# Kernel optimization log

Measured on AMD Instinct MI355X. Metric: run time of the kernel, lower is better.

## Reference

```python
import jax, jax.numpy as jnp
import numpy as np

HEAD_NUM = 8
EMB = 256
HEAD_SIZE = EMB // HEAD_NUM
POS_LEN = 128
ROPE_BASE = 100.0
LN_EPS = 1e-5
SOFTPICK_EPS = 1e-6


def _rope_tables():
    inv_freq = 1.0 / ROPE_BASE ** (jnp.arange(0, HEAD_SIZE, 2, dtype=jnp.float32) / HEAD_SIZE)
    t = jnp.arange(POS_LEN, dtype=jnp.float32)
    freqs = jnp.einsum('i,j->ij', t, inv_freq)          # [W, hs/2]
    freqs = jnp.concatenate([freqs, freqs], axis=-1)     # [W, hs]
    return jnp.sin(freqs), jnp.cos(freqs)


def _apply_rope(e, sin, cos):
    # e: [..., W, hs]; sin/cos: [W, hs]
    h = HEAD_SIZE // 2
    rot = jnp.concatenate([-e[..., h:], e[..., :h]], axis=-1)
    return e * cos + rot * sin


def _layernorm(x, g, b):
    mu = jnp.mean(x, axis=-1, keepdims=True)
    var = jnp.mean(jnp.square(x - mu), axis=-1, keepdims=True)
    return (x - mu) * jax.lax.rsqrt(var + LN_EPS) * g + b


def _softpick(x):
    m = jnp.max(x, axis=-1, keepdims=True)
    e = jnp.exp(x - m) - jnp.exp(-m)
    return jax.nn.relu(e) / (jnp.sum(jnp.abs(e), axis=-1, keepdims=True) + SOFTPICK_EPS)


def setup_inputs() -> dict:
    key = jax.random.key(0)
    ks = jax.random.split(key, 12)
    B, C, H, W = 4, EMB, 256, 128
    hn, hs = HEAD_NUM, HEAD_SIZE
    s = 0.02
    return {
        'left': jax.random.normal(ks[0], (B, C, H, W), jnp.float32),
        'right': jax.random.normal(ks[1], (B, C, H, W), jnp.float32),
        'qw': jax.random.normal(ks[2], (hn, hs, hs), jnp.float32) * s,   # grouped 1x1 conv weights
        'kw': jax.random.normal(ks[3], (hn, hs, hs), jnp.float32) * s,
        'vw': jax.random.normal(ks[4], (hn, hs, hs), jnp.float32) * s,
        'proj_w': jax.random.normal(ks[5], (C, C), jnp.float32) * s,
        'proj_b': jnp.zeros((C,), jnp.float32),
        'ln1_g': jnp.ones((C,), jnp.float32),
        'ln1_b': jnp.zeros((C,), jnp.float32),
        'ln2_g': jnp.ones((C,), jnp.float32),
        'ln2_b': jnp.zeros((C,), jnp.float32),
        'w1': jax.random.normal(ks[6], (C, 4 * C), jnp.float32) * s,
        'b1': jnp.zeros((4 * C,), jnp.float32),
        'w2': jax.random.normal(ks[7], (4 * C, C), jnp.float32) * s,
        'b2': jnp.zeros((C,), jnp.float32),
    }


def reference(left, right, qw, kw, vw, proj_w, proj_b,
              ln1_g, ln1_b, ln2_g, ln2_b, w1, b1, w2, b2):
    B, C, H, W = left.shape
    hn, hs = HEAD_NUM, HEAD_SIZE
    scale = hs ** -0.5
    sin, cos = _rope_tables()  # [W, hs]

    def grouped_proj(x, w):
        # grouped 1x1 conv -> per-head matmul; out [B, H, hn, W, hs]
        xr = x.reshape(B, hn, hs, H, W)
        return jnp.einsum('bgihw,goi->bhgwo', xr, w)

    q = _apply_rope(grouped_proj(left, qw), sin, cos)
    k = _apply_rope(grouped_proj(right, kw), sin, cos)
    v = grouped_proj(right, vw)

    att = _softpick(jnp.einsum('bhgqd,bhgkd->bhgqk', q, k) * scale)  # [B,H,hn,W,W]
    out = jnp.einsum('bhgqk,bhgkd->bhqgd', att, v).reshape(B, H, W, C)

    x1 = _layernorm(out @ proj_w + proj_b + jnp.transpose(left, (0, 2, 3, 1)), ln1_g, ln1_b)
    ffn = jax.nn.gelu(x1 @ w1 + b1, approximate=False) @ w2 + b2
    return _layernorm(ffn + x1, ln2_g, ln2_b)
```

## Files before the change

kernel.cpp:

```cpp
#include <hip/hip_runtime.h>
#include <hip/hip_bf16.h>

#define DEV __device__ __forceinline__

typedef __attribute__((ext_vector_type(8))) short bf16x8_t;
typedef __attribute__((ext_vector_type(4))) float f32x4_t;

constexpr int cB = 4, cC = 256, cH = 256, cW = 128, cHN = 8, cHS = 32;
constexpr int cM = cB * cH * cW;

DEV float bfu(unsigned int b16) { union { unsigned int u; float f; } v; v.u = b16 << 16; return v.f; }
DEV unsigned short f2bb(float f) { union { __hip_bfloat16 h; unsigned short u; } v; v.h = __float2bfloat16(f); return v.u; }
DEV unsigned int pk2(float a, float b) { return (unsigned)f2bb(a) | ((unsigned)f2bb(b) << 16); }

#define GLOAD_LDS16(g, l) \
  __builtin_amdgcn_global_load_lds((const __attribute__((address_space(1))) void*)(g), \
                                   (__attribute__((address_space(3))) void*)(l), 16, 0, 0)

DEV float gelu_fast(float v) {
  float ax = fabsf(v) * 0.7071067811865475f;
  float t = __builtin_amdgcn_rcpf(1.0f + 0.3275911f * ax);
  float poly = ((((1.061405429f * t - 1.453152027f) * t + 1.421413741f) * t
                 - 0.284496736f) * t + 0.254829592f) * t;
  float e = __expf(-ax * ax);
  float erfv = 1.0f - poly * e;
  float phi = 0.5f + 0.5f * copysignf(erfv, v);
  return v * phi;
}

__global__ __launch_bounds__(256) void transpose_bf16(const float* __restrict__ src,
                                                      __hip_bfloat16* __restrict__ dst,
                                                      int R, int Ccol) {
  int idx = blockIdx.x * 256 + threadIdx.x;
  if (idx < R * Ccol) {
    int r = idx / Ccol, c = idx - r * Ccol;
    dst[c * R + r] = __float2bfloat16(src[idx]);
  }
}

__global__ __launch_bounds__(256) void transpose_perm_fp8(const float* __restrict__ src,
                                                          unsigned char* __restrict__ dst,
                                                          int R, int Ccol) {
  int idx = blockIdx.x * 256 + threadIdx.x;
  if (idx < R * Ccol) {
    int r = idx / Ccol, c = idx - r * Ccol;
    int pk = (r & ~255) | ((r & 15) << 4) | ((r >> 4) & 15);
    int u = __builtin_amdgcn_cvt_pk_fp8_f32(src[idx] * 64.0f, 0.0f, 0, false);
    dst[(size_t)c * R + pk] = (unsigned char)(u & 0xff);
  }
}

__global__ __launch_bounds__(256) void rope_init(float2* __restrict__ tab) {
  int i = blockIdx.x * 256 + threadIdx.x;
  int w = i >> 4, c = i & 15;
  float inv = expf((float)c * -0.28782313662425572f);
  float ang = (float)w * inv;
  tab[i] = make_float2(sinf(ang), cosf(ang));
}

constexpr int XL_OFF = 0, XR_OFF = 10240, WQ_OFF = 20480, WK_OFF = 23040, WV_OFF = 25600;
constexpr int QS_OFF = 28160, KS_OFF = 38400, VT_OFF = 0, P_OFF = 10240;
constexpr int SMEM_BYTES = 48640;

__global__ __launch_bounds__(256) void attn_mfma(
    const float* __restrict__ left, const float* __restrict__ right,
    const float* __restrict__ qw, const float* __restrict__ kw, const float* __restrict__ vw,
    const float2* __restrict__ rope,
    __hip_bfloat16* __restrict__ att_out)
{
  __shared__ __align__(16) char smem[SMEM_BYTES];

  const int t = threadIdx.x;
  const int g = blockIdx.x & 7;
  const int h = (blockIdx.x >> 3) & 255;
  const int b = blockIdx.x >> 11;
  const size_t HW = (size_t)cH * cW;

  {
    const float* lb = left  + ((size_t)(b * cC + g * cHS) * cH + h) * cW;
    const float* rb = right + ((size_t)(b * cC + g * cHS) * cH + h) * cW;
    int w = t & 127, ih = (t >> 7) * 16;
    unsigned short* xlrow = (unsigned short*)(smem + XL_OFF) + w * 40 + ih;
    unsigned short* xrrow = (unsigned short*)(smem + XR_OFF) + w * 40 + ih;
#pragma unroll
    for (int i = 0; i < 16; i += 2) {
      float a0 = lb[(size_t)(ih + i) * HW + w], a1 = lb[(size_t)(ih + i + 1) * HW + w];
      *(unsigned int*)(xlrow + i) = pk2(a0, a1);
      float c0 = rb[(size_t)(ih + i) * HW + w], c1 = rb[(size_t)(ih + i + 1) * HW + w];
      *(unsigned int*)(xrrow + i) = pk2(c0, c1);
    }
    int o = t >> 3, i0 = (t & 7) * 4;
    {
      float4 v4 = *(const float4*)(qw + g * 1024 + t * 4);
      unsigned short* dst = (unsigned short*)(smem + WQ_OFF) + o * 40 + i0;
      *(unsigned int*)(dst) = pk2(v4.x, v4.y); *(unsigned int*)(dst + 2) = pk2(v4.z, v4.w);
    }
    {
      float4 v4 = *(const float4*)(kw + g * 1024 + t * 4);
      unsigned short* dst = (unsigned short*)(smem + WK_OFF) + o * 40 + i0;
      *(unsigned int*)(dst) = pk2(v4.x, v4.y); *(unsigned int*)(dst + 2) = pk2(v4.z, v4.w);
    }
    {
      float4 v4 = *(const float4*)(vw + g * 1024 + t * 4);
      unsigned short* dst = (unsigned short*)(smem + WV_OFF) + o * 40 + i0;
      *(unsigned int*)(dst) = pk2(v4.x, v4.y); *(unsigned int*)(dst + 2) = pk2(v4.z, v4.w);
    }
  }
  __syncthreads();

  const int lane = t & 63, wid = t >> 6;
  const int c = lane & 15, q4 = lane >> 4;
  const int wbase = wid * 32;
  const f32x4_t zero = {0.f, 0.f, 0.f, 0.f};

  bf16x8_t a_xl[2], a_xr[2];
#pragma unroll
  for (int sub = 0; sub < 2; ++sub) {
    a_xl[sub] = *(const bf16x8_t*)(smem + XL_OFF + (wbase + sub * 16 + c) * 80 + q4 * 16);
    a_xr[sub] = *(const bf16x8_t*)(smem + XR_OFF + (wbase + sub * 16 + c) * 80 + q4 * 16);
  }
  f32x4_t qacc[2][2], kacc[2][2];
#pragma unroll
  for (int ot = 0; ot < 2; ++ot) {
    bf16x8_t bq = *(const bf16x8_t*)(smem + WQ_OFF + (ot * 16 + c) * 80 + q4 * 16);
    bf16x8_t bk = *(const bf16x8_t*)(smem + WK_OFF + (ot * 16 + c) * 80 + q4 * 16);
#pragma unroll
    for (int sub = 0; sub < 2; ++sub) {
      qacc[sub][ot] = __builtin_amdgcn_mfma_f32_16x16x32_bf16(a_xl[sub], bq, zero, 0, 0, 0);
      kacc[sub][ot] = __builtin_amdgcn_mfma_f32_16x16x32_bf16(a_xr[sub], bk, zero, 0, 0, 0);
    }
  }
  {
    const float scale = 0.17677669529663687f;
    unsigned short* qsp = (unsigned short*)(smem + QS_OFF);
    unsigned short* ksp = (unsigned short*)(smem + KS_OFF);
#pragma unroll
    for (int sub = 0; sub < 2; ++sub)
#pragma unroll
      for (int r = 0; r < 4; ++r) {
        int w = wbase + sub * 16 + q4 * 4 + r;
        float2 sc = rope[w * 16 + c];
        float sn = sc.x, cs = sc.y;
        float q0 = qacc[sub][0][r], q1 = qacc[sub][1][r];
        qsp[w * 40 + c]      = f2bb((q0 * cs - q1 * sn) * scale);
        qsp[w * 40 + c + 16] = f2bb((q1 * cs + q0 * sn) * scale);
        float k0 = kacc[sub][0][r], k1 = kacc[sub][1][r];
        ksp[w * 40 + c]      = f2bb(k0 * cs - k1 * sn);
        ksp[w * 40 + c + 16] = f2bb(k1 * cs + k0 * sn);
      }
  }
  __syncthreads();

  {
    f32x4_t vacc[2][2];
#pragma unroll
    for (int dt = 0; dt < 2; ++dt) {
      bf16x8_t awv = *(const bf16x8_t*)(smem + WV_OFF + (dt * 16 + c) * 80 + q4 * 16);
#pragma unroll
      for (int sub = 0; sub < 2; ++sub)
        vacc[dt][sub] = __builtin_amdgcn_mfma_f32_16x16x32_bf16(awv, a_xr[sub], zero, 0, 0, 0);
    }
    unsigned short* vtp = (unsigned short*)(smem + VT_OFF);
#pragma unroll
    for (int dt = 0; dt < 2; ++dt)
#pragma unroll
      for (int r = 0; r < 4; ++r) {
        int d = dt * 16 + q4 * 4 + r;
        *(unsigned int*)(vtp + d * 136 + c * 8 + wid * 2) = pk2(vacc[dt][0][r], vacc[dt][1][r]);
      }
  }

  bf16x8_t aq0 = *(const bf16x8_t*)(smem + QS_OFF + (wbase + c) * 80 + q4 * 16);
  bf16x8_t aq1 = *(const bf16x8_t*)(smem + QS_OFF + (wbase + 16 + c) * 80 + q4 * 16);
  f32x4_t sac[2][8];
#pragma unroll
  for (int kt = 0; kt < 8; ++kt) {
    bf16x8_t bk = *(const bf16x8_t*)(smem + KS_OFF + (kt * 16 + c) * 80 + q4 * 16);
    sac[0][kt] = __builtin_amdgcn_mfma_f32_16x16x32_bf16(aq0, bk, zero, 0, 0, 0);
    sac[1][kt] = __builtin_amdgcn_mfma_f32_16x16x32_bf16(aq1, bk, zero, 0, 0, 0);
  }

  float dinv_[2][4];
#pragma unroll
  for (int sub = 0; sub < 2; ++sub)
#pragma unroll
    for (int r = 0; r < 4; ++r) {
      float m = sac[sub][0][r];
#pragma unroll
      for (int kt = 1; kt < 8; ++kt) m = fmaxf(m, sac[sub][kt][r]);
      m = fmaxf(m, __shfl_xor(m, 1));
      m = fmaxf(m, __shfl_xor(m, 2));
      m = fmaxf(m, __shfl_xor(m, 4));
      m = fmaxf(m, __shfl_xor(m, 8));
      float em = __expf(-m);
      float ss = 0.f;
#pragma unroll
      for (int kt = 0; kt < 8; ++kt) {
        float e = __expf(sac[sub][kt][r] - m) - em;
        sac[sub][kt][r] = fmaxf(e, 0.f);
        ss += fabsf(e);
      }
      ss += __shfl_xor(ss, 1);
      ss += __shfl_xor(ss, 2);
      ss += __shfl_xor(ss, 4);
      ss += __shfl_xor(ss, 8);
      dinv_[sub][r] = 1.0f / (ss + 1e-6f);
    }
  __syncthreads();

  {
    unsigned short* pp = (unsigned short*)(smem + P_OFF);
#pragma unroll
    for (int sub = 0; sub < 2; ++sub)
#pragma unroll
      for (int r = 0; r < 4; ++r) {
        int w = wbase + sub * 16 + q4 * 4 + r;
        float dv = dinv_[sub][r];
        uint4 u;
        u.x = pk2(sac[sub][0][r] * dv, sac[sub][1][r] * dv);
        u.y = pk2(sac[sub][2][r] * dv, sac[sub][3][r] * dv);
        u.z = pk2(sac[sub][4][r] * dv, sac[sub][5][r] * dv);
        u.w = pk2(sac[sub][6][r] * dv, sac[sub][7][r] * dv);
        *(uint4*)(pp + w * 136 + c * 8) = u;
      }
  }
  f32x4_t oacc[2][2] = {{zero, zero}, {zero, zero}};
#pragma unroll
  for (int ks = 0; ks < 4; ++ks) {
    bf16x8_t ap0 = *(const bf16x8_t*)(smem + P_OFF + (wbase + c) * 272 + ks * 64 + q4 * 16);
    bf16x8_t ap1 = *(const bf16x8_t*)(smem + P_OFF + (wbase + 16 + c) * 272 + ks * 64 + q4 * 16);
    bf16x8_t bv0 = *(const bf16x8_t*)(smem + VT_OFF + (c) * 272 + ks * 64 + q4 * 16);
    bf16x8_t bv1 = *(const bf16x8_t*)(smem + VT_OFF + (16 + c) * 272 + ks * 64 + q4 * 16);
    oacc[0][0] = __builtin_amdgcn_mfma_f32_16x16x32_bf16(ap0, bv0, oacc[0][0], 0, 0, 0);
    oacc[0][1] = __builtin_amdgcn_mfma_f32_16x16x32_bf16(ap0, bv1, oacc[0][1], 0, 0, 0);
    oacc[1][0] = __builtin_amdgcn_mfma_f32_16x16x32_bf16(ap1, bv0, oacc[1][0], 0, 0, 0);
    oacc[1][1] = __builtin_amdgcn_mfma_f32_16x16x32_bf16(ap1, bv1, oacc[1][1], 0, 0, 0);
  }
  {
    __hip_bfloat16* ob = att_out + ((size_t)(b * cH + h) * cW) * cC + g * cHS;
#pragma unroll
    for (int sub = 0; sub < 2; ++sub)
#pragma unroll
      for (int dt = 0; dt < 2; ++dt)
#pragma unroll
        for (int r = 0; r < 4; ++r) {
          int w = wbase + sub * 16 + q4 * 4 + r;
          ob[(size_t)w * cC + dt * 16 + c] = __float2bfloat16(oacc[sub][dt][r]);
        }
  }
}

__global__ __launch_bounds__(256, 2) void proj_gemm_ln(
    const __hip_bfloat16* __restrict__ A, const __hip_bfloat16* __restrict__ Bt,
    const float* __restrict__ bias, const float* __restrict__ leftres,
    const float* __restrict__ g, const float* __restrict__ be,
    __hip_bfloat16* __restrict__ outp)
{
  constexpr int KK = 256;
  __shared__ __align__(16) char smem[73728];
  const int t = threadIdx.x, lane = t & 63, wid = t >> 6;
  const int c = lane & 15, q4 = lane >> 4;
  const int m0 = blockIdx.x * 128;
  const int wr = wid * 32;
  const f32x4_t zero = {0.f, 0.f, 0.f, 0.f};

  f32x4_t acc[2][16];
#pragma unroll
  for (int fi = 0; fi < 2; ++fi)
#pragma unroll
    for (int fj = 0; fj < 16; ++fj) acc[fi][fj] = zero;

  auto stage = [&](int buf, int k0) {
    char* As = smem + buf * 24576;
    char* Bs = As + 8192;
#pragma unroll
    for (int i = 0; i < 2; ++i) {
      int chunk = (wid * 2 + i);
      int row = chunk * 16 + (lane >> 2);
      int sw = (((lane & 3) ^ ((row >> 1) & 3))) * 8;
      GLOAD_LDS16(A + (size_t)(m0 + row) * KK + k0 + sw, As + chunk * 1024);
    }
#pragma unroll
    for (int i = 0; i < 4; ++i) {
      int chunk = (wid * 4 + i);
      int row = chunk * 16 + (lane >> 2);
      int sw = (((lane & 3) ^ ((row >> 1) & 3))) * 8;
      GLOAD_LDS16(Bt + (size_t)row * KK + k0 + sw, Bs + chunk * 1024);
    }
  };

  constexpr int NK = KK >> 5;
  stage(0, 0);
  stage(1, 32);
  for (int tt = 0; tt < NK; ++tt) {
    if (tt + 2 < NK) {
      stage((tt + 2) % 3, (tt + 2) << 5);
      asm volatile("s_waitcnt vmcnt(12)" ::: "memory");
    } else if (tt + 1 < NK) {
      asm volatile("s_waitcnt vmcnt(6)" ::: "memory");
    } else {
      asm volatile("s_waitcnt vmcnt(0)" ::: "memory");
    }
    __builtin_amdgcn_s_barrier();
    __builtin_amdgcn_sched_barrier(0);
    char* As = smem + (tt % 3) * 24576;
    char* Bs = As + 8192;
    int ra0 = wr + c, ra1 = wr + 16 + c;
    bf16x8_t af0 = *(const bf16x8_t*)(As + ra0 * 64 + ((q4 ^ ((ra0 >> 1) & 3)) * 16));
    bf16x8_t af1 = *(const bf16x8_t*)(As + ra1 * 64 + ((q4 ^ ((ra1 >> 1) & 3)) * 16));
#pragma unroll
    for (int fj = 0; fj < 16; ++fj) {
      int rb = fj * 16 + c;
      bf16x8_t bf = *(const bf16x8_t*)(Bs + rb * 64 + ((q4 ^ ((rb >> 1) & 3)) * 16));
      acc[0][fj] = __builtin_amdgcn_mfma_f32_16x16x32_bf16(af0, bf, acc[0][fj], 0, 0, 0);
      acc[1][fj] = __builtin_amdgcn_mfma_f32_16x16x32_bf16(af1, bf, acc[1][fj], 0, 0, 0);
    }
    __builtin_amdgcn_sched_barrier(0);
    __builtin_amdgcn_s_barrier();
  }

  {
    const int b_ = m0 >> 15, h_ = (m0 >> 7) & 255;
#pragma unroll
    for (int fj = 0; fj < 16; ++fj) {
      int n = fj * 16 + c;
      float bv = bias[n];
#pragma unroll
      for (int fi = 0; fi < 2; ++fi) {
        int w0 = wr + fi * 16 + q4 * 4;
        float4 lr = *(const float4*)(leftres + (((size_t)b_ * 256 + n) * 256 + h_) * 128 + w0);
        float la[4] = {lr.x, lr.y, lr.z, lr.w};
#pragma unroll
        for (int r = 0; r < 4; ++r) acc[fi][fj][r] += bv + la[r];
      }
    }
  }

  float mu[2][4], rs[2][4];
#pragma unroll
  for (int fi = 0; fi < 2; ++fi)
#pragma unroll
    for (int r = 0; r < 4; ++r) {
      float s = 0.f;
#pragma unroll
      for (int fj = 0; fj < 16; ++fj) s += acc[fi][fj][r];
      s += __shfl_xor(s, 1); s += __shfl_xor(s, 2); s += __shfl_xor(s, 4); s += __shfl_xor(s, 8);
      float m_ = s * (1.0f / 256.0f);
      float sq = 0.f;
#pragma unroll
      for (int fj = 0; fj < 16; ++fj) { float d = acc[fi][fj][r] - m_; sq += d * d; }
      sq += __shfl_xor(sq, 1); sq += __shfl_xor(sq, 2); sq += __shfl_xor(sq, 4); sq += __shfl_xor(sq, 8);
      mu[fi][r] = m_;
      rs[fi][r] = rsqrtf(sq * (1.0f / 256.0f) + 1e-5f);
    }
#pragma unroll
  for (int fj = 0; fj < 16; ++fj) {
    int n = fj * 16 + c;
    float gv = g[n], bev = be[n];
#pragma unroll
    for (int fi = 0; fi < 2; ++fi)
#pragma unroll
      for (int r = 0; r < 4; ++r) {
        int row = wr + fi * 16 + q4 * 4 + r;
        outp[(size_t)(m0 + row) * 256 + n] =
            __float2bfloat16((acc[fi][fj][r] - mu[fi][r]) * rs[fi][r] * gv + bev);
      }
  }
}

__global__ __launch_bounds__(256, 2) void ffn1_wide(
    const __hip_bfloat16* __restrict__ A, const __hip_bfloat16* __restrict__ Bt,
    const float* __restrict__ bias, unsigned char* __restrict__ outb)
{
  constexpr int KK = 256, N = 1024;
  __shared__ __align__(16) char smem[73728];
  const int t = threadIdx.x, lane = t & 63, wid = t >> 6;
  const int c = lane & 15, q4 = lane >> 4;
  const int mb = blockIdx.x & 1023, nc = blockIdx.x >> 10;
  const int m0 = mb * 128, n0 = nc * 256;
  const int wr = wid * 32;
  const f32x4_t zero = {0.f, 0.f, 0.f, 0.f};

  f32x4_t acc[2][16];
#pragma unroll
  for (int fi = 0; fi < 2; ++fi)
#pragma unroll
    for (int fj = 0; fj < 16; ++fj) acc[fi][fj] = zero;

  const __hip_bfloat16* Bbase = Bt + (size_t)n0 * KK;

  auto stage = [&](int buf, int k0) {
    char* As = smem + buf * 24576;
    char* Bs = As + 8192;
#pragma unroll
    for (int i = 0; i < 2; ++i) {
      int chunk = (wid * 2 + i);
      int row = chunk * 16 + (lane >> 2);
      int sw = (((lane & 3) ^ ((row >> 1) & 3))) * 8;
      GLOAD_LDS16(A + (size_t)(m0 + row) * KK + k0 + sw, As + chunk * 1024);
    }
#pragma unroll
    for (int i = 0; i < 4; ++i) {
      int chunk = (wid * 4 + i);
      int row = chunk * 16 + (lane >> 2);
      int sw = (((lane & 3) ^ ((row >> 1) & 3))) * 8;
      GLOAD_LDS16(Bbase + (size_t)row * KK + k0 + sw, Bs + chunk * 1024);
    }
  };

  constexpr int NK = KK >> 5;
  stage(0, 0);
  stage(1, 32);
  for (int tt = 0; tt < NK; ++tt) {
    if (tt + 2 < NK) {
      stage((tt + 2) % 3, (tt + 2) << 5);
      asm volatile("s_waitcnt vmcnt(12)" ::: "memory");
    } else if (tt + 1 < NK) {
      asm volatile("s_waitcnt vmcnt(6)" ::: "memory");
    } else {
      asm volatile("s_waitcnt vmcnt(0)" ::: "memory");
    }
    __builtin_amdgcn_s_barrier();
    __builtin_amdgcn_sched_barrier(0);
    char* As = smem + (tt % 3) * 24576;
    char* Bs = As + 8192;
    int ra0 = wr + c, ra1 = wr + 16 + c;
    bf16x8_t af0 = *(const bf16x8_t*)(As + ra0 * 64 + ((q4 ^ ((ra0 >> 1) & 3)) * 16));
    bf16x8_t af1 = *(const bf16x8_t*)(As + ra1 * 64 + ((q4 ^ ((ra1 >> 1) & 3)) * 16));
#pragma unroll
    for (int fj = 0; fj < 16; ++fj) {
      int rb = fj * 16 + c;
      bf16x8_t bf = *(const bf16x8_t*)(Bs + rb * 64 + ((q4 ^ ((rb >> 1) & 3)) * 16));
      acc[0][fj] = __builtin_amdgcn_mfma_f32_16x16x32_bf16(af0, bf, acc[0][fj], 0, 0, 0);
      acc[1][fj] = __builtin_amdgcn_mfma_f32_16x16x32_bf16(af1, bf, acc[1][fj], 0, 0, 0);
    }
    __builtin_amdgcn_sched_barrier(0);
    __builtin_amdgcn_s_barrier();
  }

  float bv[16];
#pragma unroll
  for (int fj = 0; fj < 16; ++fj) bv[fj] = bias[n0 + fj * 16 + c];
  unsigned char* obase = outb + (size_t)(m0 + wr + q4 * 4) * N + n0 + c * 16;
#pragma unroll
  for (int fi = 0; fi < 2; ++fi)
#pragma unroll
    for (int r = 0; r < 4; ++r) {
      uint4 u;
      unsigned int* up = (unsigned int*)&u;
#pragma unroll
      for (int p = 0; p < 4; ++p) {
        float v0 = gelu_fast(acc[fi][4 * p + 0][r] + bv[4 * p + 0]) * 64.0f;
        float v1 = gelu_fast(acc[fi][4 * p + 1][r] + bv[4 * p + 1]) * 64.0f;
        float v2 = gelu_fast(acc[fi][4 * p + 2][r] + bv[4 * p + 2]) * 64.0f;
        float v3 = gelu_fast(acc[fi][4 * p + 3][r] + bv[4 * p + 3]) * 64.0f;
        int w = __builtin_amdgcn_cvt_pk_fp8_f32(v0, v1, 0, false);
        w = __builtin_amdgcn_cvt_pk_fp8_f32(v2, v3, w, true);
        up[p] = (unsigned)w;
      }
      *(uint4*)(obase + (size_t)(fi * 16 + r) * N) = u;
    }
}

__global__ __launch_bounds__(256, 2) void ffn2_ln(
    const unsigned char* __restrict__ A, const unsigned char* __restrict__ Bt,
    const float* __restrict__ bias, const __hip_bfloat16* __restrict__ resbf,
    const float* __restrict__ g, const float* __restrict__ be,
    float* __restrict__ outp)
{
  constexpr int KK = 1024;
  __shared__ __align__(16) char smem[73728];
  const int t = threadIdx.x, lane = t & 63, wid = t >> 6;
  const int c = lane & 15, q4 = lane >> 4;
  const int m0 = blockIdx.x * 128;
  const int wr = wid * 32;
  const f32x4_t zero = {0.f, 0.f, 0.f, 0.f};

  f32x4_t acc[2][16];
#pragma unroll
  for (int fi = 0; fi < 2; ++fi)
#pragma unroll
    for (int fj = 0; fj < 16; ++fj) acc[fi][fj] = zero;

  auto stage = [&](int buf, int k0) {
    char* As = smem + buf * 24576;
    char* Bs = As + 8192;
#pragma unroll
    for (int i = 0; i < 2; ++i) {
      int chunk = (wid * 2 + i);
      int row = chunk * 16 + (lane >> 2);
      int sw = (((lane & 3) ^ ((row >> 1) & 3))) * 16;
      GLOAD_LDS16(A + (size_t)(m0 + row) * KK + k0 + sw, As + chunk * 1024);
    }
#pragma unroll
    for (int i = 0; i < 4; ++i) {
      int chunk = (wid * 4 + i);
      int row = chunk * 16 + (lane >> 2);
      int sw = (((lane & 3) ^ ((row >> 1) & 3))) * 16;
      GLOAD_LDS16(Bt + (size_t)row * KK + k0 + sw, Bs + chunk * 1024);
    }
  };

  constexpr int NK = 16;
  stage(0, 0);
  stage(1, 64);
  const int sl = (c >> 1) & 3;
  const int koff0 = ((((q4 >> 1)) ^ sl) << 4) | ((q4 & 1) << 3);
  const int koff1 = (((2 | (q4 >> 1)) ^ sl) << 4) | ((q4 & 1) << 3);
  for (int tt = 0; tt < NK; ++tt) {
    if (tt + 2 < NK) {
      stage((tt + 2) % 3, (tt + 2) << 6);
      asm volatile("s_waitcnt vmcnt(12)" ::: "memory");
    } else if (tt + 1 < NK) {
      asm volatile("s_waitcnt vmcnt(6)" ::: "memory");
    } else {
      asm volatile("s_waitcnt vmcnt(0)" ::: "memory");
    }
    __builtin_amdgcn_s_barrier();
    __builtin_amdgcn_sched_barrier(0);
    char* As = smem + (tt % 3) * 24576;
    char* Bs = As + 8192;
    const char* arow0 = As + (wr + c) * 64;
    const char* arow1 = As + (wr + 16 + c) * 64;
    long a00 = *(const long*)(arow0 + koff0);
    long a01 = *(const long*)(arow0 + koff1);
    long a10 = *(const long*)(arow1 + koff0);
    long a11 = *(const long*)(arow1 + koff1);
#pragma unroll
    for (int fj = 0; fj < 16; ++fj) {
      const char* brow = Bs + (fj * 16 + c) * 64;
      long b0 = *(const long*)(brow + koff0);
      long b1 = *(const long*)(brow + koff1);
      acc[0][fj] = __builtin_amdgcn_mfma_f32_16x16x32_fp8_fp8(a00, b0, acc[0][fj], 0, 0, 0);
      acc[0][fj] = __builtin_amdgcn_mfma_f32_16x16x32_fp8_fp8(a01, b1, acc[0][fj], 0, 0, 0);
      acc[1][fj] = __builtin_amdgcn_mfma_f32_16x16x32_fp8_fp8(a10, b0, acc[1][fj], 0, 0, 0);
      acc[1][fj] = __builtin_amdgcn_mfma_f32_16x16x32_fp8_fp8(a11, b1, acc[1][fj], 0, 0, 0);
    }
    __builtin_amdgcn_sched_barrier(0);
    __builtin_amdgcn_s_barrier();
  }

#pragma unroll
  for (int fj = 0; fj < 16; ++fj) {
    int n = fj * 16 + c;
    float bv = bias[n];
#pragma unroll
    for (int fi = 0; fi < 2; ++fi)
#pragma unroll
      for (int r = 0; r < 4; ++r) {
        int row = wr + fi * 16 + q4 * 4 + r;
        acc[fi][fj][r] = acc[fi][fj][r] * 0.000244140625f + bv +
                         __bfloat162float(resbf[(size_t)(m0 + row) * 256 + n]);
      }
  }

  float mu[2][4], rs[2][4];
#pragma unroll
  for (int fi = 0; fi < 2; ++fi)
#pragma unroll
    for (int r = 0; r < 4; ++r) {
      float s = 0.f;
#pragma unroll
      for (int fj = 0; fj < 16; ++fj) s += acc[fi][fj][r];
      s += __shfl_xor(s, 1); s += __shfl_xor(s, 2); s += __shfl_xor(s, 4); s += __shfl_xor(s, 8);
      float m_ = s * (1.0f / 256.0f);
      float sq = 0.f;
#pragma unroll
      for (int fj = 0; fj < 16; ++fj) { float d = acc[fi][fj][r] - m_; sq += d * d; }
      sq += __shfl_xor(sq, 1); sq += __shfl_xor(sq, 2); sq += __shfl_xor(sq, 4); sq += __shfl_xor(sq, 8);
      mu[fi][r] = m_;
      rs[fi][r] = rsqrtf(sq * (1.0f / 256.0f) + 1e-5f);
    }
#pragma unroll
  for (int fj = 0; fj < 16; ++fj) {
    int n = fj * 16 + c;
    float gv = g[n], bev = be[n];
#pragma unroll
    for (int fi = 0; fi < 2; ++fi)
#pragma unroll
      for (int r = 0; r < 4; ++r) {
        int row = wr + fi * 16 + q4 * 4 + r;
        outp[(size_t)(m0 + row) * 256 + n] =
            (acc[fi][fj][r] - mu[fi][r]) * rs[fi][r] * gv + bev;
      }
  }
}

extern "C" void kernel_launch(void* const* d_in, const int* in_sizes, int n_in,
                              void* d_out, int out_size, void* d_ws, size_t ws_size,
                              hipStream_t stream) {
  const float* left   = (const float*)d_in[0];
  const float* right  = (const float*)d_in[1];
  const float* qw     = (const float*)d_in[2];
  const float* kw     = (const float*)d_in[3];
  const float* vw     = (const float*)d_in[4];
  const float* proj_w = (const float*)d_in[5];
  const float* proj_b = (const float*)d_in[6];
  const float* ln1_g  = (const float*)d_in[7];
  const float* ln1_b  = (const float*)d_in[8];
  const float* ln2_g  = (const float*)d_in[9];
  const float* ln2_b  = (const float*)d_in[10];
  const float* w1     = (const float*)d_in[11];
  const float* b1     = (const float*)d_in[12];
  const float* w2     = (const float*)d_in[13];
  const float* b2     = (const float*)d_in[14];

  char* ws = (char*)d_ws;
  __hip_bfloat16* att_out = (__hip_bfloat16*)ws;
  __hip_bfloat16* x1      = (__hip_bfloat16*)(ws + 67108864);
  unsigned char*  hidden  = (unsigned char*)(ws + 134217728);
  float2*         rope    = (float2*)(ws + 301989888);
  __hip_bfloat16* pwT     = (__hip_bfloat16*)(ws + 402653184);
  __hip_bfloat16* w1T     = pwT + 65536;
  unsigned char*  w2T     = (unsigned char*)(w1T + 262144);

  transpose_bf16<<<256, 256, 0, stream>>>(proj_w, pwT, 256, 256);
  transpose_bf16<<<1024, 256, 0, stream>>>(w1, w1T, 256, 1024);
  transpose_perm_fp8<<<1024, 256, 0, stream>>>(w2, w2T, 1024, 256);
  rope_init<<<8, 256, 0, stream>>>(rope);

  attn_mfma<<<cB * cH * cHN, 256, 0, stream>>>(left, right, qw, kw, vw, rope, att_out);

  proj_gemm_ln<<<cM / 128, 256, 0, stream>>>(att_out, pwT, proj_b, left, ln1_g, ln1_b, x1);
  ffn1_wide<<<4096, 256, 0, stream>>>(x1, w1T, b1, hidden);
  ffn2_ln<<<cM / 128, 256, 0, stream>>>(hidden, w2T, b2, x1, ln2_g, ln2_b, (float*)d_out);
}
```

Measured before the change: 411.7 us.

## Load attention inputs directly into registers, use FP8 for PV, remap FFN1 blocks per XCD

```diff
diff --git a/kernel.cpp b/kernel.cpp
--- a/kernel.cpp
+++ b/kernel.cpp
@@ -58,9 +58,9 @@
   tab[i] = make_float2(sinf(ang), cosf(ang));
 }
 
-constexpr int XL_OFF = 0, XR_OFF = 10240, WQ_OFF = 20480, WK_OFF = 23040, WV_OFF = 25600;
-constexpr int QS_OFF = 28160, KS_OFF = 38400, VT_OFF = 0, P_OFF = 10240;
-constexpr int SMEM_BYTES = 48640;
+constexpr int WQ_OFF = 0, WK_OFF = 2560, WV_OFF = 5120, QS_OFF = 7680, KS_OFF = 17920;
+constexpr int VT_OFF = 28160, P_OFF = 0;
+constexpr int SMEM_BYTES = 32512;
 
 __global__ __launch_bounds__(256) void attn_mfma(
     const float* __restrict__ left, const float* __restrict__ right,
@@ -76,19 +76,35 @@
   const int b = blockIdx.x >> 11;
   const size_t HW = (size_t)cH * cW;
 
+  const int lane = t & 63, wid = t >> 6;
+  const int c = lane & 15, q4 = lane >> 4;
+  const int wbase = wid * 32;
+  const f32x4_t zero = {0.f, 0.f, 0.f, 0.f};
+
+  const float* lb = left  + ((size_t)(b * cC + g * cHS) * cH + h) * cW;
+  const float* rb = right + ((size_t)(b * cC + g * cHS) * cH + h) * cW;
+
+  bf16x8_t a_xl[2], a_xr[2];
+#pragma unroll
+  for (int sub = 0; sub < 2; ++sub) {
+    int w = wbase + sub * 16 + c;
+    float xl[8], xr[8];
+#pragma unroll
+    for (int e = 0; e < 8; ++e) {
+      xl[e] = lb[(size_t)(q4 * 8 + e) * HW + w];
+      xr[e] = rb[(size_t)(q4 * 8 + e) * HW + w];
+    }
+    union { bf16x8_t v; unsigned int u[4]; } ul, ur;
+#pragma unroll
+    for (int p = 0; p < 4; ++p) {
+      ul.u[p] = pk2(xl[2 * p], xl[2 * p + 1]);
+      ur.u[p] = pk2(xr[2 * p], xr[2 * p + 1]);
+    }
+    a_xl[sub] = ul.v;
+    a_xr[sub] = ur.v;
+  }
+
   {
-    const float* lb = left  + ((size_t)(b * cC + g * cHS) * cH + h) * cW;
-    const float* rb = right + ((size_t)(b * cC + g * cHS) * cH + h) * cW;
-    int w = t & 127, ih = (t >> 7) * 16;
-    unsigned short* xlrow = (unsigned short*)(smem + XL_OFF) + w * 40 + ih;
-    unsigned short* xrrow = (unsigned short*)(smem + XR_OFF) + w * 40 + ih;
-#pragma unroll
-    for (int i = 0; i < 16; i += 2) {
-      float a0 = lb[(size_t)(ih + i) * HW + w], a1 = lb[(size_t)(ih + i + 1) * HW + w];
-      *(unsigned int*)(xlrow + i) = pk2(a0, a1);
-      float c0 = rb[(size_t)(ih + i) * HW + w], c1 = rb[(size_t)(ih + i + 1) * HW + w];
-      *(unsigned int*)(xrrow + i) = pk2(c0, c1);
-    }
     int o = t >> 3, i0 = (t & 7) * 4;
     {
       float4 v4 = *(const float4*)(qw + g * 1024 + t * 4);
@@ -108,17 +124,6 @@
   }
   __syncthreads();
 
-  const int lane = t & 63, wid = t >> 6;
-  const int c = lane & 15, q4 = lane >> 4;
-  const int wbase = wid * 32;
-  const f32x4_t zero = {0.f, 0.f, 0.f, 0.f};
-
-  bf16x8_t a_xl[2], a_xr[2];
-#pragma unroll
-  for (int sub = 0; sub < 2; ++sub) {
-    a_xl[sub] = *(const bf16x8_t*)(smem + XL_OFF + (wbase + sub * 16 + c) * 80 + q4 * 16);
-    a_xr[sub] = *(const bf16x8_t*)(smem + XR_OFF + (wbase + sub * 16 + c) * 80 + q4 * 16);
-  }
   f32x4_t qacc[2][2], kacc[2][2];
 #pragma unroll
   for (int ot = 0; ot < 2; ++ot) {
@@ -160,13 +165,15 @@
       for (int sub = 0; sub < 2; ++sub)
         vacc[dt][sub] = __builtin_amdgcn_mfma_f32_16x16x32_bf16(awv, a_xr[sub], zero, 0, 0, 0);
     }
-    unsigned short* vtp = (unsigned short*)(smem + VT_OFF);
+    unsigned char* vtp = (unsigned char*)(smem + VT_OFF);
 #pragma unroll
     for (int dt = 0; dt < 2; ++dt)
 #pragma unroll
       for (int r = 0; r < 4; ++r) {
         int d = dt * 16 + q4 * 4 + r;
-        *(unsigned int*)(vtp + d * 136 + c * 8 + wid * 2) = pk2(vacc[dt][0][r], vacc[dt][1][r]);
+        int u = __builtin_amdgcn_cvt_pk_fp8_f32(vacc[dt][0][r] * 16.0f,
+                                                vacc[dt][1][r] * 16.0f, 0, false);
+        *(unsigned short*)(vtp + d * 136 + c * 8 + wid * 2) = (unsigned short)(u & 0xffff);
       }
   }
 
@@ -209,32 +216,33 @@
   __syncthreads();
 
   {
-    unsigned short* pp = (unsigned short*)(smem + P_OFF);
+    unsigned char* pp = (unsigned char*)(smem + P_OFF);
 #pragma unroll
     for (int sub = 0; sub < 2; ++sub)
 #pragma unroll
       for (int r = 0; r < 4; ++r) {
         int w = wbase + sub * 16 + q4 * 4 + r;
-        float dv = dinv_[sub][r];
-        uint4 u;
-        u.x = pk2(sac[sub][0][r] * dv, sac[sub][1][r] * dv);
-        u.y = pk2(sac[sub][2][r] * dv, sac[sub][3][r] * dv);
-        u.z = pk2(sac[sub][4][r] * dv, sac[sub][5][r] * dv);
-        u.w = pk2(sac[sub][6][r] * dv, sac[sub][7][r] * dv);
-        *(uint4*)(pp + w * 136 + c * 8) = u;
-      }
-  }
+        float s16 = dinv_[sub][r] * 16.0f;
+        int u0 = __builtin_amdgcn_cvt_pk_fp8_f32(sac[sub][0][r] * s16, sac[sub][1][r] * s16, 0, false);
+        u0 = __builtin_amdgcn_cvt_pk_fp8_f32(sac[sub][2][r] * s16, sac[sub][3][r] * s16, u0, true);
+        int u1 = __builtin_amdgcn_cvt_pk_fp8_f32(sac[sub][4][r] * s16, sac[sub][5][r] * s16, 0, false);
+        u1 = __builtin_amdgcn_cvt_pk_fp8_f32(sac[sub][6][r] * s16, sac[sub][7][r] * s16, u1, true);
+        uint2 u; u.x = (unsigned)u0; u.y = (unsigned)u1;
+        *(uint2*)(pp + w * 136 + c * 8) = u;
+      }
+  }
+
   f32x4_t oacc[2][2] = {{zero, zero}, {zero, zero}};
 #pragma unroll
   for (int ks = 0; ks < 4; ++ks) {
-    bf16x8_t ap0 = *(const bf16x8_t*)(smem + P_OFF + (wbase + c) * 272 + ks * 64 + q4 * 16);
-    bf16x8_t ap1 = *(const bf16x8_t*)(smem + P_OFF + (wbase + 16 + c) * 272 + ks * 64 + q4 * 16);
-    bf16x8_t bv0 = *(const bf16x8_t*)(smem + VT_OFF + (c) * 272 + ks * 64 + q4 * 16);
-    bf16x8_t bv1 = *(const bf16x8_t*)(smem + VT_OFF + (16 + c) * 272 + ks * 64 + q4 * 16);
-    oacc[0][0] = __builtin_amdgcn_mfma_f32_16x16x32_bf16(ap0, bv0, oacc[0][0], 0, 0, 0);
-    oacc[0][1] = __builtin_amdgcn_mfma_f32_16x16x32_bf16(ap0, bv1, oacc[0][1], 0, 0, 0);
-    oacc[1][0] = __builtin_amdgcn_mfma_f32_16x16x32_bf16(ap1, bv0, oacc[1][0], 0, 0, 0);
-    oacc[1][1] = __builtin_amdgcn_mfma_f32_16x16x32_bf16(ap1, bv1, oacc[1][1], 0, 0, 0);
+    long ap0 = *(const long*)(smem + P_OFF + (wbase + c) * 136 + ks * 32 + q4 * 8);
+    long ap1 = *(const long*)(smem + P_OFF + (wbase + 16 + c) * 136 + ks * 32 + q4 * 8);
+    long bv0 = *(const long*)(smem + VT_OFF + (c) * 136 + ks * 32 + q4 * 8);
+    long bv1 = *(const long*)(smem + VT_OFF + (16 + c) * 136 + ks * 32 + q4 * 8);
+    oacc[0][0] = __builtin_amdgcn_mfma_f32_16x16x32_fp8_fp8(ap0, bv0, oacc[0][0], 0, 0, 0);
+    oacc[0][1] = __builtin_amdgcn_mfma_f32_16x16x32_fp8_fp8(ap0, bv1, oacc[0][1], 0, 0, 0);
+    oacc[1][0] = __builtin_amdgcn_mfma_f32_16x16x32_fp8_fp8(ap1, bv0, oacc[1][0], 0, 0, 0);
+    oacc[1][1] = __builtin_amdgcn_mfma_f32_16x16x32_fp8_fp8(ap1, bv1, oacc[1][1], 0, 0, 0);
   }
   {
     __hip_bfloat16* ob = att_out + ((size_t)(b * cH + h) * cW) * cC + g * cHS;
@@ -245,9 +253,106 @@
 #pragma unroll
         for (int r = 0; r < 4; ++r) {
           int w = wbase + sub * 16 + q4 * 4 + r;
-          ob[(size_t)w * cC + dt * 16 + c] = __float2bfloat16(oacc[sub][dt][r]);
+          ob[(size_t)w * cC + dt * 16 + c] = __float2bfloat16(oacc[sub][dt][r] * 0.00390625f);
         }
   }
+}
+
+__global__ __launch_bounds__(256, 2) void ffn1_wide(
+    const __hip_bfloat16* __restrict__ A, const __hip_bfloat16* __restrict__ Bt,
+    const float* __restrict__ bias, unsigned char* __restrict__ outb)
+{
+  constexpr int KK = 256, N = 1024;
+  __shared__ __align__(16) char smem[73728];
+  const int t = threadIdx.x, lane = t & 63, wid = t >> 6;
+  const int c = lane & 15, q4 = lane >> 4;
+  const int id = blockIdx.x;
+  const int xcd = id & 7, k = id >> 3;
+  const int nc = k & 3, mbl = k >> 2;
+  const int m0 = (xcd * 128 + mbl) * 128;
+  const int n0 = nc * 256;
+  const int wr = wid * 32;
+  const f32x4_t zero = {0.f, 0.f, 0.f, 0.f};
+
+  f32x4_t acc[2][16];
+#pragma unroll
+  for (int fi = 0; fi < 2; ++fi)
+#pragma unroll
+    for (int fj = 0; fj < 16; ++fj) acc[fi][fj] = zero;
+
+  const __hip_bfloat16* Bbase = Bt + (size_t)n0 * KK;
+
+  auto stage = [&](int buf, int k0) {
+    char* As = smem + buf * 24576;
+    char* Bs = As + 8192;
+#pragma unroll
+    for (int i = 0; i < 2; ++i) {
+      int chunk = (wid * 2 + i);
+      int row = chunk * 16 + (lane >> 2);
+      int sw = (((lane & 3) ^ ((row >> 1) & 3))) * 8;
+      GLOAD_LDS16(A + (size_t)(m0 + row) * KK + k0 + sw, As + chunk * 1024);
+    }
+#pragma unroll
+    for (int i = 0; i < 4; ++i) {
+      int chunk = (wid * 4 + i);
+      int row = chunk * 16 + (lane >> 2);
+      int sw = (((lane & 3) ^ ((row >> 1) & 3))) * 8;
+      GLOAD_LDS16(Bbase + (size_t)row * KK + k0 + sw, Bs + chunk * 1024);
+    }
+  };
+
+  constexpr int NK = KK >> 5;
+  stage(0, 0);
+  stage(1, 32);
+  for (int tt = 0; tt < NK; ++tt) {
+    if (tt + 2 < NK) {
+      stage((tt + 2) % 3, (tt + 2) << 5);
+      asm volatile("s_waitcnt vmcnt(12)" ::: "memory");
+    } else if (tt + 1 < NK) {
+      asm volatile("s_waitcnt vmcnt(6)" ::: "memory");
+    } else {
+      asm volatile("s_waitcnt vmcnt(0)" ::: "memory");
+    }
+    __builtin_amdgcn_s_barrier();
+    __builtin_amdgcn_sched_barrier(0);
+    char* As = smem + (tt % 3) * 24576;
+    char* Bs = As + 8192;
+    int ra0 = wr + c, ra1 = wr + 16 + c;
+    bf16x8_t af0 = *(const bf16x8_t*)(As + ra0 * 64 + ((q4 ^ ((ra0 >> 1) & 3)) * 16));
+    bf16x8_t af1 = *(const bf16x8_t*)(As + ra1 * 64 + ((q4 ^ ((ra1 >> 1) & 3)) * 16));
+#pragma unroll
+    for (int fj = 0; fj < 16; ++fj) {
+      int rb = fj * 16 + c;
+      bf16x8_t bf = *(const bf16x8_t*)(Bs + rb * 64 + ((q4 ^ ((rb >> 1) & 3)) * 16));
+      acc[0][fj] = __builtin_amdgcn_mfma_f32_16x16x32_bf16(af0, bf, acc[0][fj], 0, 0, 0);
+      acc[1][fj] = __builtin_amdgcn_mfma_f32_16x16x32_bf16(af1, bf, acc[1][fj], 0, 0, 0);
+    }
+    __builtin_amdgcn_sched_barrier(0);
+    __builtin_amdgcn_s_barrier();
+  }
+
+  float bv[16];
+#pragma unroll
+  for (int fj = 0; fj < 16; ++fj) bv[fj] = bias[n0 + fj * 16 + c];
+  unsigned char* obase = outb + (size_t)(m0 + wr + q4 * 4) * N + n0 + c * 16;
+#pragma unroll
+  for (int fi = 0; fi < 2; ++fi)
+#pragma unroll
+    for (int r = 0; r < 4; ++r) {
+      uint4 u;
+      unsigned int* up = (unsigned int*)&u;
+#pragma unroll
+      for (int p = 0; p < 4; ++p) {
+        float v0 = gelu_fast(acc[fi][4 * p + 0][r] + bv[4 * p + 0]) * 64.0f;
+        float v1 = gelu_fast(acc[fi][4 * p + 1][r] + bv[4 * p + 1]) * 64.0f;
+        float v2 = gelu_fast(acc[fi][4 * p + 2][r] + bv[4 * p + 2]) * 64.0f;
+        float v3 = gelu_fast(acc[fi][4 * p + 3][r] + bv[4 * p + 3]) * 64.0f;
+        int w = __builtin_amdgcn_cvt_pk_fp8_f32(v0, v1, 0, false);
+        w = __builtin_amdgcn_cvt_pk_fp8_f32(v2, v3, w, true);
+        up[p] = (unsigned)w;
+      }
+      *(uint4*)(obase + (size_t)(fi * 16 + r) * N) = u;
+    }
 }
 
 __global__ __launch_bounds__(256, 2) void proj_gemm_ln(
@@ -366,100 +471,6 @@
             __float2bfloat16((acc[fi][fj][r] - mu[fi][r]) * rs[fi][r] * gv + bev);
       }
   }
-}
-
-__global__ __launch_bounds__(256, 2) void ffn1_wide(
-    const __hip_bfloat16* __restrict__ A, const __hip_bfloat16* __restrict__ Bt,
-    const float* __restrict__ bias, unsigned char* __restrict__ outb)
-{
-  constexpr int KK = 256, N = 1024;
-  __shared__ __align__(16) char smem[73728];
-  const int t = threadIdx.x, lane = t & 63, wid = t >> 6;
-  const int c = lane & 15, q4 = lane >> 4;
-  const int mb = blockIdx.x & 1023, nc = blockIdx.x >> 10;
-  const int m0 = mb * 128, n0 = nc * 256;
-  const int wr = wid * 32;
-  const f32x4_t zero = {0.f, 0.f, 0.f, 0.f};
-
-  f32x4_t acc[2][16];
-#pragma unroll
-  for (int fi = 0; fi < 2; ++fi)
-#pragma unroll
-    for (int fj = 0; fj < 16; ++fj) acc[fi][fj] = zero;
-
-  const __hip_bfloat16* Bbase = Bt + (size_t)n0 * KK;
-
-  auto stage = [&](int buf, int k0) {
-    char* As = smem + buf * 24576;
-    char* Bs = As + 8192;
-#pragma unroll
-    for (int i = 0; i < 2; ++i) {
-      int chunk = (wid * 2 + i);
-      int row = chunk * 16 + (lane >> 2);
-      int sw = (((lane & 3) ^ ((row >> 1) & 3))) * 8;
-      GLOAD_LDS16(A + (size_t)(m0 + row) * KK + k0 + sw, As + chunk * 1024);
-    }
-#pragma unroll
-    for (int i = 0; i < 4; ++i) {
-      int chunk = (wid * 4 + i);
-      int row = chunk * 16 + (lane >> 2);
-      int sw = (((lane & 3) ^ ((row >> 1) & 3))) * 8;
-      GLOAD_LDS16(Bbase + (size_t)row * KK + k0 + sw, Bs + chunk * 1024);
-    }
-  };
-
-  constexpr int NK = KK >> 5;
-  stage(0, 0);
-  stage(1, 32);
-  for (int tt = 0; tt < NK; ++tt) {
-    if (tt + 2 < NK) {
-      stage((tt + 2) % 3, (tt + 2) << 5);
-      asm volatile("s_waitcnt vmcnt(12)" ::: "memory");
-    } else if (tt + 1 < NK) {
-      asm volatile("s_waitcnt vmcnt(6)" ::: "memory");
-    } else {
-      asm volatile("s_waitcnt vmcnt(0)" ::: "memory");
-    }
-    __builtin_amdgcn_s_barrier();
-    __builtin_amdgcn_sched_barrier(0);
-    char* As = smem + (tt % 3) * 24576;
-    char* Bs = As + 8192;
-    int ra0 = wr + c, ra1 = wr + 16 + c;
-    bf16x8_t af0 = *(const bf16x8_t*)(As + ra0 * 64 + ((q4 ^ ((ra0 >> 1) & 3)) * 16));
-    bf16x8_t af1 = *(const bf16x8_t*)(As + ra1 * 64 + ((q4 ^ ((ra1 >> 1) & 3)) * 16));
-#pragma unroll
-    for (int fj = 0; fj < 16; ++fj) {
-      int rb = fj * 16 + c;
-      bf16x8_t bf = *(const bf16x8_t*)(Bs + rb * 64 + ((q4 ^ ((rb >> 1) & 3)) * 16));
-      acc[0][fj] = __builtin_amdgcn_mfma_f32_16x16x32_bf16(af0, bf, acc[0][fj], 0, 0, 0);
-      acc[1][fj] = __builtin_amdgcn_mfma_f32_16x16x32_bf16(af1, bf, acc[1][fj], 0, 0, 0);
-    }
-    __builtin_amdgcn_sched_barrier(0);
-    __builtin_amdgcn_s_barrier();
-  }
-
-  float bv[16];
-#pragma unroll
-  for (int fj = 0; fj < 16; ++fj) bv[fj] = bias[n0 + fj * 16 + c];
-  unsigned char* obase = outb + (size_t)(m0 + wr + q4 * 4) * N + n0 + c * 16;
-#pragma unroll
-  for (int fi = 0; fi < 2; ++fi)
-#pragma unroll
-    for (int r = 0; r < 4; ++r) {
-      uint4 u;
-      unsigned int* up = (unsigned int*)&u;
-#pragma unroll
-      for (int p = 0; p < 4; ++p) {
-        float v0 = gelu_fast(acc[fi][4 * p + 0][r] + bv[4 * p + 0]) * 64.0f;
-        float v1 = gelu_fast(acc[fi][4 * p + 1][r] + bv[4 * p + 1]) * 64.0f;
-        float v2 = gelu_fast(acc[fi][4 * p + 2][r] + bv[4 * p + 2]) * 64.0f;
-        float v3 = gelu_fast(acc[fi][4 * p + 3][r] + bv[4 * p + 3]) * 64.0f;
-        int w = __builtin_amdgcn_cvt_pk_fp8_f32(v0, v1, 0, false);
-        w = __builtin_amdgcn_cvt_pk_fp8_f32(v2, v3, w, true);
-        up[p] = (unsigned)w;
-      }
-      *(uint4*)(obase + (size_t)(fi * 16 + r) * N) = u;
-    }
 }
 
 __global__ __launch_bounds__(256, 2) void ffn2_ln(
```

Measured after the change: 408.3 us. About the same (-0.8%).
